# Kernel tuning notes

Hardware: AMD Instinct MI355X
Metric: run time of the kernel (lower is better)

## Reference

```python
import jax, jax.numpy as jnp
import numpy as np

B, C, NS, NT = 8, 256, 16384, 2048
KQ = 64            # self-attention key/query dim
D = 64             # cond_conv_feat_dim
W0, W1, W2 = D * D, D * D, D * 1   # dynamic weight sizes (predict_mask=True)
B0, B1, B2 = D, D, 1
CTRL = W0 + W1 + W2 + B0 + B1 + B2  # 8385


def setup_inputs() -> dict:
    key = jax.random.key(0)
    ks = jax.random.split(key, 9)
    return {
        "scene_feat": jax.random.normal(ks[0], (B, C, NS), jnp.float32),
        "template_feat": jax.random.normal(ks[1], (B, C, NT), jnp.float32),
        # SelfAttention 1x1-conv (= linear over channels) weights
        "q_w": jax.random.normal(ks[2], (KQ, C), jnp.float32) * 0.02,
        "k_w": jax.random.normal(ks[3], (KQ, C), jnp.float32) * 0.02,
        "v_w": jax.random.normal(ks[4], (C, C), jnp.float32) * 0.02,
        # projection head of SimpleAggregator: Conv1d(3*C -> D, k=1) + ReLU
        "proj_w": jax.random.normal(ks[5], (D, 3 * C), jnp.float32) * 0.02,
        "proj_b": jnp.zeros((D,), jnp.float32),
        # controller head: Linear(C -> CTRL), init normal(std=0.01), bias 0
        "ctrl_w": jax.random.normal(ks[6], (CTRL, C), jnp.float32) * 0.01,
        "ctrl_b": jnp.zeros((CTRL,), jnp.float32),
    }


def _self_attention(x, q_w, k_w, v_w):
    # x: [B, C, N] -> [B, C_out, N]
    q = jnp.einsum("kc,bcn->bnk", q_w, x)          # [B, N, KQ]
    k = jnp.einsum("kc,bcn->bkn", k_w, x)          # [B, KQ, N]
    v = jnp.einsum("oc,bcn->bno", v_w, x)          # [B, N, C_out]
    attn = jax.nn.softmax(jnp.einsum("bnk,bkm->bnm", q / jnp.sqrt(jnp.float32(KQ)), k), axis=-1)
    y = jnp.einsum("bnm,bmo->bon", attn, v)        # [B, C_out, N]
    return y


def reference(scene_feat, template_feat, q_w, k_w, v_w, proj_w, proj_b, ctrl_w, ctrl_b):
    # ---- SimpleAggregator (self-attention on template inside) ----
    t_sa = _self_attention(template_feat, q_w, k_w, v_w)       # [B, C, NT]
    t_max = jnp.max(t_sa, axis=-1, keepdims=True)              # [B, C, 1]
    aggr = jnp.concatenate(
        [scene_feat - t_max, scene_feat * t_max, scene_feat], axis=1
    )                                                          # [B, 3C, NS]
    x = jax.nn.relu(jnp.einsum("oc,bcn->bon", proj_w, aggr) + proj_b[None, :, None])  # [B, D, NS]

    # ---- controller head on ORIGINAL template_feat max-pooled ----
    pooled = jnp.max(template_feat, axis=-1)                   # [B, C]
    params = pooled @ ctrl_w.T + ctrl_b                        # [B, CTRL]

    # parse_dynamic_params: splits = weights then biases
    o = 0
    w0 = params[:, o:o + W0].reshape(B, D, D); o += W0
    w1 = params[:, o:o + W1].reshape(B, D, D); o += W1
    w2 = params[:, o:o + W2].reshape(B, 1, D); o += W2
    b0 = params[:, o:o + B0]; o += B0
    b1 = params[:, o:o + B1]; o += B1
    b2 = params[:, o:o + B2]

    # per-sample dynamic 1x1 convs (groups=batch trick == batched GEMM)
    x = jax.nn.relu(jnp.einsum("boi,bin->bon", w0, x) + b0[:, :, None])
    x = jax.nn.relu(jnp.einsum("boi,bin->bon", w1, x) + b1[:, :, None])
    x = jnp.einsum("boi,bin->bon", w2, x) + b2[:, :, None]    # [B, 1, NS], no relu (mask layer)
    return x.reshape(B, NS)
```

## Files before the change

### kernel.cpp

```cpp
#include <hip/hip_runtime.h>


typedef __attribute__((ext_vector_type(8))) short short8;
typedef __attribute__((ext_vector_type(4))) short short4v;
typedef __attribute__((ext_vector_type(4))) float f32x4;

__device__ __forceinline__ unsigned short f2bf(float f){
  unsigned u = __float_as_uint(f);
  u += 0x7FFFu + ((u >> 16) & 1u);
  return (unsigned short)(u >> 16);
}
__device__ __forceinline__ unsigned fenc(float f){
  unsigned u = __float_as_uint(f);
  return (u & 0x80000000u) ? ~u : (u | 0x80000000u);
}
__device__ __forceinline__ float fdec(unsigned k){
  unsigned u = (k & 0x80000000u) ? (k & 0x7FFFFFFFu) : ~k;
  return __uint_as_float(u);
}

__global__ __launch_bounds__(256) void k0w(const float* __restrict__ qw,
    const float* __restrict__ kw, const float* __restrict__ vw,
    unsigned short* __restrict__ Wbf, unsigned* __restrict__ tmaxe,
    unsigned* __restrict__ pooledEnc){
  if (blockIdx.x == 0){
    const unsigned ninf = fenc(-3.0e38f);
    for (int i = threadIdx.x; i < 2048; i += 256){
      tmaxe[i] = 0u;
      pooledEnc[i] = ninf;
    }
  }
  const int e = (blockIdx.x * 256 + threadIdx.x) * 4;
  const int row = e >> 8, c = e & 255;
  const float* src;
  float scl = 1.0f;
  if (row < 64){ src = qw + row * 256 + c; scl = 0.125f; }
  else if (row < 128){ src = kw + (row - 64) * 256 + c; }
  else { src = vw + (row - 128) * 256 + c; }
  float4 v = *(const float4*)src;
  short4v o;
  o[0] = (short)f2bf(v.x * scl); o[1] = (short)f2bf(v.y * scl);
  o[2] = (short)f2bf(v.z * scl); o[3] = (short)f2bf(v.w * scl);
  *(short4v*)(Wbf + e) = o;
}

__global__ __launch_bounds__(256) void k0_tt(const float* __restrict__ T,
    unsigned short* __restrict__ Tt, unsigned* __restrict__ pooledEnc){
  const int b = blockIdx.x, nt = blockIdx.y, ct = blockIdx.z;
  const int n0 = nt * 128, c0 = ct * 32;
  const int tid = threadIdx.x;
  __shared__ float Ls[32][129];
  const int cr = tid >> 3, nq = tid & 7;
  const float* src = T + ((size_t)b * 256 + c0 + cr) * 2048 + n0 + nq * 16;
  float4 v0 = ((const float4*)src)[0];
  float4 v1 = ((const float4*)src)[1];
  float4 v2 = ((const float4*)src)[2];
  float4 v3 = ((const float4*)src)[3];
  float mx = fmaxf(fmaxf(fmaxf(v0.x, v0.y), fmaxf(v0.z, v0.w)),
                   fmaxf(fmaxf(v1.x, v1.y), fmaxf(v1.z, v1.w)));
  mx = fmaxf(mx, fmaxf(fmaxf(fmaxf(v2.x, v2.y), fmaxf(v2.z, v2.w)),
                       fmaxf(fmaxf(v3.x, v3.y), fmaxf(v3.z, v3.w))));
  mx = fmaxf(mx, __shfl_xor(mx, 1));
  mx = fmaxf(mx, __shfl_xor(mx, 2));
  mx = fmaxf(mx, __shfl_xor(mx, 4));
  if (nq == 0) atomicMax(&pooledEnc[b * 256 + c0 + cr], fenc(mx));
  float* lr = &Ls[cr][nq * 16];
  *(float4*)lr = v0; *(float4*)(lr + 4) = v1;
  *(float4*)(lr + 8) = v2; *(float4*)(lr + 12) = v3;
  __syncthreads();
  const int nr = tid >> 1, ch = tid & 1;
  unsigned short ob[16];
  #pragma unroll
  for (int j = 0; j < 16; j++) ob[j] = f2bf(Ls[ch * 16 + j][nr]);
  unsigned short* dst = Tt + ((size_t)b * 2048 + n0 + nr) * 256 + c0 + ch * 16;
  *(short8*)dst = *(short8*)&ob[0];
  *(short8*)(dst + 8) = *(short8*)&ob[8];
}

__global__ __launch_bounds__(256) void k2_qkv(const unsigned short* __restrict__ Wbf,
    const unsigned short* __restrict__ Tt,
    unsigned short* __restrict__ qo, unsigned short* __restrict__ ko,
    unsigned short* __restrict__ vt){
  const int wg = blockIdx.x;
  const int b = wg & 7, nt = wg >> 3;
  const int n0 = nt * 32;
  const int tid = threadIdx.x, lane = tid & 63, w = tid >> 6;
  const int l15 = lane & 15, g = lane >> 4;
  const unsigned short* Tb = Tt + (size_t)b * 2048 * 256;

  f32x4 aqk[2][2], av[4][2];
  #pragma unroll
  for (int i = 0; i < 2; i++)
    #pragma unroll
    for (int nf = 0; nf < 2; nf++) aqk[i][nf] = (f32x4){0.f,0.f,0.f,0.f};
  #pragma unroll
  for (int j = 0; j < 4; j++)
    #pragma unroll
    for (int nf = 0; nf < 2; nf++) av[j][nf] = (f32x4){0.f,0.f,0.f,0.f};

  #pragma unroll 2
  for (int kc = 0; kc < 8; kc++){
    short8 bfr[2];
    #pragma unroll
    for (int nf = 0; nf < 2; nf++)
      bfr[nf] = *(const short8*)(Tb + (size_t)(n0 + nf * 16 + l15) * 256 + kc * 32 + g * 8);
    short8 aq[2];
    #pragma unroll
    for (int i = 0; i < 2; i++)
      aq[i] = *(const short8*)(Wbf + (size_t)((2 * w + i) * 16 + l15) * 256 + kc * 32 + g * 8);
    short8 afv[4];
    #pragma unroll
    for (int j = 0; j < 4; j++)
      afv[j] = *(const short8*)(Wbf + (size_t)(128 + (4 * w + j) * 16 + l15) * 256 + kc * 32 + g * 8);
    #pragma unroll
    for (int i = 0; i < 2; i++)
      #pragma unroll
      for (int nf = 0; nf < 2; nf++)
        aqk[i][nf] = __builtin_amdgcn_mfma_f32_16x16x32_bf16(aq[i], bfr[nf], aqk[i][nf], 0, 0, 0);
    #pragma unroll
    for (int j = 0; j < 4; j++)
      #pragma unroll
      for (int nf = 0; nf < 2; nf++)
        av[j][nf] = __builtin_amdgcn_mfma_f32_16x16x32_bf16(bfr[nf], afv[j], av[j][nf], 0, 0, 0);
  }
  unsigned short* qk = (w < 2) ? qo : ko;
  #pragma unroll
  for (int i = 0; i < 2; i++)
    #pragma unroll
    for (int nf = 0; nf < 2; nf++){
      int n = n0 + nf * 16 + l15;
      int cbase = (w & 1) * 32 + i * 16 + g * 4;
      short4v pk;
      #pragma unroll
      for (int r = 0; r < 4; r++) pk[r] = (short)f2bf(aqk[i][nf][r]);
      *(short4v*)(qk + ((size_t)b * 2048 + n) * 64 + cbase) = pk;
    }
  #pragma unroll
  for (int j = 0; j < 4; j++)
    #pragma unroll
    for (int nf = 0; nf < 2; nf++){
      int o = (4 * w + j) * 16 + l15;
      int nb2 = n0 + nf * 16 + g * 4;
      short4v pv;
      #pragma unroll
      for (int r = 0; r < 4; r++) pv[r] = (short)f2bf(av[j][nf][r]);
      *(short4v*)(vt + ((size_t)b * 256 + o) * 2048 + nb2) = pv;
    }
}

__global__ __launch_bounds__(256) void k3_params(const unsigned* __restrict__ pooledEnc,
    const float* __restrict__ cw, const float* __restrict__ cb,
    float* __restrict__ params){
  __shared__ float P[8 * 256];
  const int tid = threadIdx.x;
  for (int i = tid; i < 2048; i += 256) P[i] = fdec(pooledEnc[i]);
  __syncthreads();
  const int w = tid >> 6, lane = tid & 63;
  const int r = blockIdx.x * 4 + w;
  if (r >= 8385) return;
  float4 c4 = ((const float4*)(cw + (size_t)r * 256))[lane];
  float bias = cb[r];
  #pragma unroll
  for (int b = 0; b < 8; b++){
    const float* pbp = P + b * 256 + lane * 4;
    float s = c4.x * pbp[0] + c4.y * pbp[1] + c4.z * pbp[2] + c4.w * pbp[3];
    #pragma unroll
    for (int d = 1; d < 64; d <<= 1) s += __shfl_xor(s, d);
    if (lane == 0) params[b * 8385 + r] = s + bias;
  }
}

__global__ __launch_bounds__(512, 4) void kA_scores(
    const unsigned short* __restrict__ Qg, const unsigned short* __restrict__ Kg,
    unsigned short* __restrict__ Pg, float* __restrict__ sbuf,
    int b0, int bshift){
  const int wg = blockIdx.x;
  const int bmask = (1 << bshift) - 1;
  const int b = b0 + (wg & bmask);
  const int q0 = (wg >> bshift) * 32;
  const int qb0 = (wg >> bshift) * 2;
  const int tid = threadIdx.x, lane = tid & 63, w = tid >> 6;
  const int l15 = lane & 15, g = lane >> 4;
  __shared__ float wsum[32][8];
  const unsigned short* Qb = Qg + (size_t)b * 2048 * 64;
  const unsigned short* Kb = Kg + (size_t)b * 2048 * 64;
  unsigned short* Pb = Pg + (size_t)(wg & bmask) * 2048 * 2048;

  short8 qf[2][2];
  #pragma unroll
  for (int qi = 0; qi < 2; qi++)
    #pragma unroll
    for (int kc = 0; kc < 2; kc++)
      qf[qi][kc] = *(const short8*)(Qb + (size_t)(q0 + qi * 16 + l15) * 64 + kc * 32 + g * 8);

  float ps[2][4];
  #pragma unroll
  for (int qi = 0; qi < 2; qi++)
    #pragma unroll
    for (int r = 0; r < 4; r++) ps[qi][r] = 0.f;

  const int wm0 = w * 256;
  for (int mt = 0; mt < 4; ++mt){
    const int mb = wm0 + mt * 64;
    short8 kf[4][2];
    #pragma unroll
    for (int mi = 0; mi < 4; mi++)
      #pragma unroll
      for (int kc = 0; kc < 2; kc++)
        kf[mi][kc] = *(const short8*)(Kb + (size_t)(mb + mi * 16 + l15) * 64 + kc * 32 + g * 8);
    #pragma unroll
    for (int qi = 0; qi < 2; qi++){
      f32x4 sa[4];
      #pragma unroll
      for (int mi = 0; mi < 4; mi++) sa[mi] = (f32x4){0.f,0.f,0.f,0.f};
      #pragma unroll
      for (int mi = 0; mi < 4; mi++)
        #pragma unroll
        for (int kc = 0; kc < 2; kc++)
          sa[mi] = __builtin_amdgcn_mfma_f32_16x16x32_bf16(qf[qi][kc], kf[mi][kc], sa[mi], 0, 0, 0);
      #pragma unroll
      for (int mi = 0; mi < 4; mi++){
        short4v pk;
        #pragma unroll
        for (int r = 0; r < 4; r++){
          float p = __expf(sa[mi][r]);
          ps[qi][r] += p;
          pk[r] = (short)f2bf(p);
        }
        *(short4v*)(Pb + ((size_t)((qb0 + qi) * 128 + w * 16 + mt * 4 + mi)) * 256 + lane * 4) = pk;
      }
    }
  }
  #pragma unroll
  for (int qi = 0; qi < 2; qi++)
    #pragma unroll
    for (int r = 0; r < 4; r++){
      float t = ps[qi][r];
      t += __shfl_xor(t, 1); t += __shfl_xor(t, 2);
      t += __shfl_xor(t, 4); t += __shfl_xor(t, 8);
      if (l15 == 0) wsum[qi * 16 + g * 4 + r][w] = t;
    }
  __syncthreads();
  if (tid < 32){
    float t = 0.f;
    #pragma unroll
    for (int i = 0; i < 8; i++) t += wsum[tid][i];
    sbuf[(size_t)b * 2048 + q0 + tid] = t;
  }
}

__global__ __launch_bounds__(256, 2) void kB_pv(
    const unsigned short* __restrict__ Pg, const unsigned short* __restrict__ Vt,
    const float* __restrict__ sbuf, unsigned* __restrict__ tmaxe,
    int b0, int bshift){
  const int wg = blockIdx.x;
  const int bmask = (1 << bshift) - 1;
  const int b = b0 + (wg & bmask);
  const int rest = wg >> bshift;
  const int oh = rest & 1;
  const int n0 = (rest >> 1) * 64;
  const int qb0 = n0 >> 4;
  const int tid = threadIdx.x, lane = tid & 63, w = tid >> 6;
  const int l15 = lane & 15, g = lane >> 4;
  __shared__ __align__(16) unsigned char smem[24576];

  const unsigned short* Pb = Pg + (size_t)(wg & bmask) * 2048 * 2048;
  const unsigned short* Vb = Vt + ((size_t)b * 256 + oh * 128) * 2048;

  f32x4 acc[4][2];
  #pragma unroll
  for (int ni = 0; ni < 4; ni++)
    #pragma unroll
    for (int oi = 0; oi < 2; oi++) acc[ni][oi] = (f32x4){0.f,0.f,0.f,0.f};

  for (int m0 = 0; m0 < 2048; m0 += 64){
    const int mb0 = m0 >> 4;
    short8 stg[6];
    #pragma unroll
    for (int k = 0; k < 6; k++){
      int d = k * 4096 + tid * 16;
      if (k < 2){
        int ti = d >> 9;
        int qi = ti >> 2, mi = ti & 3;
        stg[k] = *(const short8*)(Pb + ((size_t)(qb0 + qi) * 128 + mb0 + mi) * 256 + ((d & 511) >> 1));
      } else {
        int dv = d - 8192;
        int row = dv >> 7;
        stg[k] = *(const short8*)(Vb + (size_t)row * 2048 + m0 + ((dv & 127) >> 1));
      }
    }
    __syncthreads();
    #pragma unroll
    for (int k = 0; k < 6; k++){
      int d = k * 4096 + tid * 16;
      if (k < 2){
        int ti = d >> 9;
        int qi = ti >> 2, mi = ti & 3;
        int lane0 = (d & 511) >> 3;
        #pragma unroll
        for (int idx = 0; idx < 8; idx++){
          int Lp = lane0 + (idx >> 2), r = idx & 3;
          int row = qi * 16 + ((Lp >> 4) << 2) + r;
          int col = mi * 16 + (Lp & 15);
          *(unsigned short*)(smem + ((row * 128 + col * 2) ^ ((row & 7) << 4))) =
              ((const unsigned short*)&stg[k])[idx];
        }
      } else {
        int dv = d - 8192;
        int row = dv >> 7;
        *(short8*)(smem + 8192 + (dv ^ ((row & 7) << 4))) = stg[k];
      }
    }
    __syncthreads();
    short8 af[4][2], bf[2][2];
    #pragma unroll
    for (int ni = 0; ni < 4; ni++)
      #pragma unroll
      for (int kc = 0; kc < 2; kc++){
        int row = ni * 16 + l15;
        af[ni][kc] = *(const short8*)(smem + ((row * 128 + kc * 64 + g * 16) ^ ((row & 7) << 4)));
      }
    #pragma unroll
    for (int oi = 0; oi < 2; oi++)
      #pragma unroll
      for (int kc = 0; kc < 2; kc++){
        int row = w * 32 + oi * 16 + l15;
        bf[oi][kc] = *(const short8*)(smem + 8192 + ((row * 128 + kc * 64 + g * 16) ^ ((row & 7) << 4)));
      }
    #pragma unroll
    for (int ni = 0; ni < 4; ni++)
      #pragma unroll
      for (int oi = 0; oi < 2; oi++)
        #pragma unroll
        for (int kc = 0; kc < 2; kc++)
          acc[ni][oi] = __builtin_amdgcn_mfma_f32_16x16x32_bf16(af[ni][kc], bf[oi][kc], acc[ni][oi], 0, 0, 0);
  }
  float inv[4][4];
  #pragma unroll
  for (int ni = 0; ni < 4; ni++)
    #pragma unroll
    for (int r = 0; r < 4; r++)
      inv[ni][r] = 1.0f / sbuf[(size_t)b * 2048 + n0 + ni * 16 + g * 4 + r];
  #pragma unroll
  for (int oi = 0; oi < 2; oi++){
    float cm = -1e30f;
    #pragma unroll
    for (int ni = 0; ni < 4; ni++)
      #pragma unroll
      for (int r = 0; r < 4; r++)
        cm = fmaxf(cm, acc[ni][oi][r] * inv[ni][r]);
    cm = fmaxf(cm, __shfl_xor(cm, 16));
    cm = fmaxf(cm, __shfl_xor(cm, 32));
    if (lane < 16)
      atomicMax(&tmaxe[b * 256 + oh * 128 + w * 32 + oi * 16 + lane], fenc(cm));
  }
}

__global__ __launch_bounds__(256) void k5_weff(const float* __restrict__ proj_w,
    const float* __restrict__ proj_b, const unsigned* __restrict__ tmaxe,
    const float* __restrict__ params, unsigned short* __restrict__ weff,
    float* __restrict__ beff, unsigned short* __restrict__ w0b,
    unsigned short* __restrict__ w1b){
  const int b = blockIdx.y, o = blockIdx.x;
  const int c = threadIdx.x;
  float t = fdec(tmaxe[b * 256 + c]);
  float p0 = proj_w[o * 768 + c];
  float p1 = proj_w[o * 768 + 256 + c];
  float p2 = proj_w[o * 768 + 512 + c];
  weff[((size_t)b * 64 + o) * 256 + c] = f2bf(p0 + p1 * t + p2);
  float s = p0 * t;
  #pragma unroll
  for (int d = 1; d < 64; d <<= 1) s += __shfl_xor(s, d);
  __shared__ float sm[4];
  if ((c & 63) == 0) sm[c >> 6] = s;
  __syncthreads();
  if (c == 0) beff[b * 64 + o] = proj_b[o] - (sm[0] + sm[1] + sm[2] + sm[3]);
  if (c < 64)        w0b[((size_t)b * 64 + o) * 64 + c] = f2bf(params[b * 8385 + o * 64 + c]);
  else if (c < 128)  w1b[((size_t)b * 64 + o) * 64 + (c - 64)] = f2bf(params[b * 8385 + 4096 + o * 64 + (c - 64)]);
}

__global__ __launch_bounds__(512) void k6_main(const float* __restrict__ Sg,
    const unsigned short* __restrict__ weff, const float* __restrict__ beff,
    const unsigned short* __restrict__ w0b, const unsigned short* __restrict__ w1b,
    const float* __restrict__ params, float* __restrict__ out){
  const int b = blockIdx.y, nt = blockIdx.x;
  const int n0 = nt * 256;
  const int tid = threadIdx.x, lane = tid & 63, w = tid >> 6;
  const int l15 = lane & 15, g = lane >> 4;
  __shared__ __align__(16) unsigned char smem[65536];
  unsigned short* H0 = (unsigned short*)smem;
  unsigned char*  Ub = smem + 32768;
  unsigned short* H1 = (unsigned short*)Ub;

  const float* Sb = Sg + (size_t)b * 256 * 16384;
  const unsigned short* We = weff + (size_t)b * 64 * 256;
  f32x4 a0[4][2];
  #pragma unroll
  for (int mi = 0; mi < 4; mi++)
    #pragma unroll
    for (int ni = 0; ni < 2; ni++) a0[mi][ni] = (f32x4){0.f,0.f,0.f,0.f};

  const int scc = tid & 31;
  const int snb = (tid >> 5) * 16;
  for (int k0 = 0; k0 < 256; k0 += 32){
    const float* src = Sb + (size_t)(k0 + scc) * 16384 + n0 + snb;
    float4 v0 = ((const float4*)src)[0];
    float4 v1 = ((const float4*)src)[1];
    float4 v2 = ((const float4*)src)[2];
    float4 v3 = ((const float4*)src)[3];
    float vals[16] = {v0.x,v0.y,v0.z,v0.w, v1.x,v1.y,v1.z,v1.w,
                      v2.x,v2.y,v2.z,v2.w, v3.x,v3.y,v3.z,v3.w};
    #pragma unroll
    for (int j = 0; j < 16; j++){
      int n = snb + j;
      unsigned byteo = ((unsigned)(n * 64 + scc * 2)) ^ ((unsigned)((n >> 1) & 3) << 4);
      *(unsigned short*)(Ub + byteo) = f2bf(vals[j]);
    }
    __syncthreads();
    short8 bf0[2];
    #pragma unroll
    for (int ni = 0; ni < 2; ni++){
      int n = w * 32 + ni * 16 + l15;
      bf0[ni] = *(const short8*)(Ub + (((unsigned)(n * 64 + g * 16)) ^ ((unsigned)((n >> 1) & 3) << 4)));
    }
    #pragma unroll
    for (int mi = 0; mi < 4; mi++){
      short8 af = *(const short8*)(We + (mi * 16 + l15) * 256 + k0 + g * 8);
      #pragma unroll
      for (int ni = 0; ni < 2; ni++)
        a0[mi][ni] = __builtin_amdgcn_mfma_f32_16x16x32_bf16(af, bf0[ni], a0[mi][ni], 0, 0, 0);
    }
    __syncthreads();
  }
  const float* be = beff + b * 64;
  #pragma unroll
  for (int mi = 0; mi < 4; mi++)
    #pragma unroll
    for (int ni = 0; ni < 2; ni++){
      int n = w * 32 + ni * 16 + l15;
      unsigned base = ((unsigned)(n * 128 + mi * 32 + g * 8)) ^ ((unsigned)((n & 7) << 4));
      unsigned short hh[4];
      #pragma unroll
      for (int r = 0; r < 4; r++){
        int o = mi * 16 + g * 4 + r;
        hh[r] = f2bf(fmaxf(a0[mi][ni][r] + be[o], 0.f));
      }
      *(unsigned*)((unsigned char*)H0 + base)     = (unsigned)hh[0] | ((unsigned)hh[1] << 16);
      *(unsigned*)((unsigned char*)H0 + base + 4) = (unsigned)hh[2] | ((unsigned)hh[3] << 16);
    }
  __syncthreads();
  f32x4 a1[4][2];
  #pragma unroll
  for (int mi = 0; mi < 4; mi++)
    #pragma unroll
    for (int ni = 0; ni < 2; ni++) a1[mi][ni] = (f32x4){0.f,0.f,0.f,0.f};
  const unsigned short* W0 = w0b + (size_t)b * 4096;
  #pragma unroll
  for (int ks = 0; ks < 2; ks++){
    short8 bfh[2];
    #pragma unroll
    for (int ni = 0; ni < 2; ni++){
      int n = w * 32 + ni * 16 + l15;
      unsigned off = ((unsigned)(n * 128 + ks * 64 + g * 16)) ^ ((unsigned)((n & 7) << 4));
      bfh[ni] = *(const short8*)((unsigned char*)H0 + off);
    }
    #pragma unroll
    for (int mi = 0; mi < 4; mi++){
      short8 af = *(const short8*)(W0 + (mi * 16 + l15) * 64 + ks * 32 + g * 8);
      #pragma unroll
      for (int ni = 0; ni < 2; ni++)
        a1[mi][ni] = __builtin_amdgcn_mfma_f32_16x16x32_bf16(af, bfh[ni], a1[mi][ni], 0, 0, 0);
    }
  }
  const float* pp = params + (size_t)b * 8385;
  const float* b0p = pp + 8256;
  #pragma unroll
  for (int mi = 0; mi < 4; mi++)
    #pragma unroll
    for (int ni = 0; ni < 2; ni++){
      int n = w * 32 + ni * 16 + l15;
      unsigned base = ((unsigned)(n * 128 + mi * 32 + g * 8)) ^ ((unsigned)((n & 7) << 4));
      unsigned short hh[4];
      #pragma unroll
      for (int r = 0; r < 4; r++){
        int o = mi * 16 + g * 4 + r;
        hh[r] = f2bf(fmaxf(a1[mi][ni][r] + b0p[o], 0.f));
      }
      *(unsigned*)((unsigned char*)H1 + base)     = (unsigned)hh[0] | ((unsigned)hh[1] << 16);
      *(unsigned*)((unsigned char*)H1 + base + 4) = (unsigned)hh[2] | ((unsigned)hh[3] << 16);
    }
  __syncthreads();
  f32x4 a2[4][2];
  #pragma unroll
  for (int mi = 0; mi < 4; mi++)
    #pragma unroll
    for (int ni = 0; ni < 2; ni++) a2[mi][ni] = (f32x4){0.f,0.f,0.f,0.f};
  const unsigned short* W1 = w1b + (size_t)b * 4096;
  #pragma unroll
  for (int ks = 0; ks < 2; ks++){
    short8 bfh[2];
    #pragma unroll
    for (int ni = 0; ni < 2; ni++){
      int n = w * 32 + ni * 16 + l15;
      unsigned off = ((unsigned)(n * 128 + ks * 64 + g * 16)) ^ ((unsigned)((n & 7) << 4));
      bfh[ni] = *(const short8*)((unsigned char*)H1 + off);
    }
    #pragma unroll
    for (int mi = 0; mi < 4; mi++){
      short8 af = *(const short8*)(W1 + (mi * 16 + l15) * 64 + ks * 32 + g * 8);
      #pragma unroll
      for (int ni = 0; ni < 2; ni++)
        a2[mi][ni] = __builtin_amdgcn_mfma_f32_16x16x32_bf16(af, bfh[ni], a2[mi][ni], 0, 0, 0);
    }
  }
  const float* b1p = pp + 8320;
  const float* w2p = pp + 8192;
  float b2v = pp[8384];
  #pragma unroll
  for (int ni = 0; ni < 2; ni++){
    float t = 0.f;
    #pragma unroll
    for (int mi = 0; mi < 4; mi++)
      #pragma unroll
      for (int r = 0; r < 4; r++){
        int o = mi * 16 + g * 4 + r;
        t += w2p[o] * fmaxf(a2[mi][ni][r] + b1p[o], 0.f);
      }
    t += __shfl_xor(t, 16);
    t += __shfl_xor(t, 32);
    if (lane < 16)
      out[(size_t)b * 16384 + n0 + w * 32 + ni * 16 + l15] = t + b2v;
  }
}

extern "C" void kernel_launch(void* const* d_in, const int* in_sizes, int n_in,
                              void* d_out, int out_size, void* d_ws, size_t ws_size,
                              hipStream_t stream){
  const float* scene = (const float*)d_in[0];
  const float* tmpl  = (const float*)d_in[1];
  const float* qw    = (const float*)d_in[2];
  const float* kw    = (const float*)d_in[3];
  const float* vw    = (const float*)d_in[4];
  const float* pw    = (const float*)d_in[5];
  const float* pb    = (const float*)d_in[6];
  const float* cw    = (const float*)d_in[7];
  const float* cb    = (const float*)d_in[8];
  float* out = (float*)d_out;
  char* ws = (char*)d_ws;

  unsigned short* Q      = (unsigned short*)(ws + 0);
  unsigned short* K      = (unsigned short*)(ws + (2u << 20));
  unsigned short* V      = (unsigned short*)(ws + (4u << 20));
  unsigned*       pooledEnc = (unsigned*)(ws + (12u << 20));
  unsigned*       tmaxe  = (unsigned*)(ws + (12u << 20) + 8192);
  float*          params = (float*)(ws + (12u << 20) + 16384);
  unsigned short* w0b    = (unsigned short*)(ws + (13u << 20));
  unsigned short* w1b    = (unsigned short*)(ws + (13u << 20) + 65536);
  unsigned short* weff   = (unsigned short*)(ws + (13u << 20) + 131072);
  float*          beff   = (float*)(ws + (13u << 20) + 131072 + 262144);
  float*          sbuf   = (float*)(ws + (14u << 20));
  unsigned short* Wbf    = (unsigned short*)(ws + (14u << 20) + 131072);
  unsigned short* Pbuf   = (unsigned short*)(ws + (16u << 20));
  unsigned short* Tt     = Pbuf;

  const size_t pPerBatch = (size_t)2048 * 2048 * 2;
  size_t avail = ws_size > (16u << 20) ? ws_size - (16u << 20) : 0;
  int nb = 8, bshift = 3;
  while (nb > 1 && (size_t)nb * pPerBatch > avail){ nb >>= 1; bshift--; }

  k0w<<<dim3(96), dim3(256), 0, stream>>>(qw, kw, vw, Wbf, tmaxe, pooledEnc);
  k0_tt<<<dim3(8, 16, 8), dim3(256), 0, stream>>>(tmpl, Tt, pooledEnc);
  k2_qkv<<<dim3(512), dim3(256), 0, stream>>>(Wbf, Tt, Q, K, V);
  k3_params<<<dim3(2097), dim3(256), 0, stream>>>(pooledEnc, cw, cb, params);
  for (int b0 = 0; b0 < 8; b0 += nb){
    kA_scores<<<dim3(64 * nb), dim3(512), 0, stream>>>(Q, K, Pbuf, sbuf, b0, bshift);
    kB_pv<<<dim3(64 * nb), dim3(256), 0, stream>>>(Pbuf, V, sbuf, tmaxe, b0, bshift);
  }
  k5_weff<<<dim3(64, 8), dim3(256), 0, stream>>>(pw, pb, tmaxe, params, weff, beff, w0b, w1b);
  k6_main<<<dim3(64, 8), dim3(512), 0, stream>>>(scene, weff, beff, w0b, w1b, params, out);
}
```

Baseline: 153.0 us.

## Double-buffer PV shared memory, merge QKV and params kernels, unroll scores loop

```diff
diff --git a/kernel.cpp b/kernel.cpp
--- a/kernel.cpp
+++ b/kernel.cpp
@@ -77,14 +77,34 @@
   *(short8*)(dst + 8) = *(short8*)&ob[8];
 }
 
-__global__ __launch_bounds__(256) void k2_qkv(const unsigned short* __restrict__ Wbf,
-    const unsigned short* __restrict__ Tt,
+__global__ __launch_bounds__(256) void k23_qkv_params(
+    const unsigned short* __restrict__ Wbf, const unsigned short* __restrict__ Tt,
     unsigned short* __restrict__ qo, unsigned short* __restrict__ ko,
-    unsigned short* __restrict__ vt){
+    unsigned short* __restrict__ vt,
+    const unsigned* __restrict__ pooledEnc, const float* __restrict__ cw,
+    const float* __restrict__ cb, float* __restrict__ params){
   const int wg = blockIdx.x;
+  const int tid = threadIdx.x, lane = tid & 63, w = tid >> 6;
+  if (wg >= 512){
+    __shared__ float P[8 * 256];
+    for (int i = tid; i < 2048; i += 256) P[i] = fdec(pooledEnc[i]);
+    __syncthreads();
+    const int r = (wg - 512) * 4 + w;
+    if (r >= 8385) return;
+    float4 c4 = ((const float4*)(cw + (size_t)r * 256))[lane];
+    float bias = cb[r];
+    #pragma unroll
+    for (int b = 0; b < 8; b++){
+      const float* pbp = P + b * 256 + lane * 4;
+      float s = c4.x * pbp[0] + c4.y * pbp[1] + c4.z * pbp[2] + c4.w * pbp[3];
+      #pragma unroll
+      for (int d = 1; d < 64; d <<= 1) s += __shfl_xor(s, d);
+      if (lane == 0) params[b * 8385 + r] = s + bias;
+    }
+    return;
+  }
   const int b = wg & 7, nt = wg >> 3;
   const int n0 = nt * 32;
-  const int tid = threadIdx.x, lane = tid & 63, w = tid >> 6;
   const int l15 = lane & 15, g = lane >> 4;
   const unsigned short* Tb = Tt + (size_t)b * 2048 * 256;
 
@@ -146,28 +166,6 @@
       for (int r = 0; r < 4; r++) pv[r] = (short)f2bf(av[j][nf][r]);
       *(short4v*)(vt + ((size_t)b * 256 + o) * 2048 + nb2) = pv;
     }
-}
-
-__global__ __launch_bounds__(256) void k3_params(const unsigned* __restrict__ pooledEnc,
-    const float* __restrict__ cw, const float* __restrict__ cb,
-    float* __restrict__ params){
-  __shared__ float P[8 * 256];
-  const int tid = threadIdx.x;
-  for (int i = tid; i < 2048; i += 256) P[i] = fdec(pooledEnc[i]);
-  __syncthreads();
-  const int w = tid >> 6, lane = tid & 63;
-  const int r = blockIdx.x * 4 + w;
-  if (r >= 8385) return;
-  float4 c4 = ((const float4*)(cw + (size_t)r * 256))[lane];
-  float bias = cb[r];
-  #pragma unroll
-  for (int b = 0; b < 8; b++){
-    const float* pbp = P + b * 256 + lane * 4;
-    float s = c4.x * pbp[0] + c4.y * pbp[1] + c4.z * pbp[2] + c4.w * pbp[3];
-    #pragma unroll
-    for (int d = 1; d < 64; d <<= 1) s += __shfl_xor(s, d);
-    if (lane == 0) params[b * 8385 + r] = s + bias;
-  }
 }
 
 __global__ __launch_bounds__(512, 4) void kA_scores(
@@ -200,6 +198,7 @@
     for (int r = 0; r < 4; r++) ps[qi][r] = 0.f;
 
   const int wm0 = w * 256;
+  #pragma unroll
   for (int mt = 0; mt < 4; ++mt){
     const int mb = wm0 + mt * 64;
     short8 kf[4][2];
@@ -262,7 +261,7 @@
   const int qb0 = n0 >> 4;
   const int tid = threadIdx.x, lane = tid & 63, w = tid >> 6;
   const int l15 = lane & 15, g = lane >> 4;
-  __shared__ __align__(16) unsigned char smem[24576];
+  __shared__ __align__(16) unsigned char smem[2][24576];
 
   const unsigned short* Pb = Pg + (size_t)(wg & bmask) * 2048 * 2048;
   const unsigned short* Vb = Vt + ((size_t)b * 256 + oh * 128) * 2048;
@@ -273,9 +272,9 @@
     #pragma unroll
     for (int oi = 0; oi < 2; oi++) acc[ni][oi] = (f32x4){0.f,0.f,0.f,0.f};
 
-  for (int m0 = 0; m0 < 2048; m0 += 64){
+  short8 stg[6];
+  auto LOADS = [&](int m0){
     const int mb0 = m0 >> 4;
-    short8 stg[6];
     #pragma unroll
     for (int k = 0; k < 6; k++){
       int d = k * 4096 + tid * 16;
@@ -289,7 +288,8 @@
         stg[k] = *(const short8*)(Vb + (size_t)row * 2048 + m0 + ((dv & 127) >> 1));
       }
     }
-    __syncthreads();
+  };
+  auto WRITES = [&](unsigned char* buf){
     #pragma unroll
     for (int k = 0; k < 6; k++){
       int d = k * 4096 + tid * 16;
@@ -302,30 +302,38 @@
           int Lp = lane0 + (idx >> 2), r = idx & 3;
           int row = qi * 16 + ((Lp >> 4) << 2) + r;
           int col = mi * 16 + (Lp & 15);
-          *(unsigned short*)(smem + ((row * 128 + col * 2) ^ ((row & 7) << 4))) =
+          *(unsigned short*)(buf + ((row * 128 + col * 2) ^ ((row & 7) << 4))) =
               ((const unsigned short*)&stg[k])[idx];
         }
       } else {
         int dv = d - 8192;
         int row = dv >> 7;
-        *(short8*)(smem + 8192 + (dv ^ ((row & 7) << 4))) = stg[k];
-      }
-    }
-    __syncthreads();
+        *(short8*)(buf + 8192 + (dv ^ ((row & 7) << 4))) = stg[k];
+      }
+    }
+  };
+
+  LOADS(0);
+  WRITES(smem[0]);
+  __syncthreads();
+
+  for (int t = 0; t < 32; ++t){
+    unsigned char* cur = smem[t & 1];
+    if (t < 31) LOADS((t + 1) * 64);
     short8 af[4][2], bf[2][2];
     #pragma unroll
     for (int ni = 0; ni < 4; ni++)
       #pragma unroll
       for (int kc = 0; kc < 2; kc++){
         int row = ni * 16 + l15;
-        af[ni][kc] = *(const short8*)(smem + ((row * 128 + kc * 64 + g * 16) ^ ((row & 7) << 4)));
+        af[ni][kc] = *(const short8*)(cur + ((row * 128 + kc * 64 + g * 16) ^ ((row & 7) << 4)));
       }
     #pragma unroll
     for (int oi = 0; oi < 2; oi++)
       #pragma unroll
       for (int kc = 0; kc < 2; kc++){
         int row = w * 32 + oi * 16 + l15;
-        bf[oi][kc] = *(const short8*)(smem + 8192 + ((row * 128 + kc * 64 + g * 16) ^ ((row & 7) << 4)));
+        bf[oi][kc] = *(const short8*)(cur + 8192 + ((row * 128 + kc * 64 + g * 16) ^ ((row & 7) << 4)));
       }
     #pragma unroll
     for (int ni = 0; ni < 4; ni++)
@@ -334,6 +342,10 @@
         #pragma unroll
         for (int kc = 0; kc < 2; kc++)
           acc[ni][oi] = __builtin_amdgcn_mfma_f32_16x16x32_bf16(af[ni][kc], bf[oi][kc], acc[ni][oi], 0, 0, 0);
+    if (t < 31){
+      WRITES(smem[(t + 1) & 1]);
+      __syncthreads();
+    }
   }
   float inv[4][4];
   #pragma unroll
@@ -570,8 +582,8 @@
 
   k0w<<<dim3(96), dim3(256), 0, stream>>>(qw, kw, vw, Wbf, tmaxe, pooledEnc);
   k0_tt<<<dim3(8, 16, 8), dim3(256), 0, stream>>>(tmpl, Tt, pooledEnc);
-  k2_qkv<<<dim3(512), dim3(256), 0, stream>>>(Wbf, Tt, Q, K, V);
-  k3_params<<<dim3(2097), dim3(256), 0, stream>>>(pooledEnc, cw, cb, params);
+  k23_qkv_params<<<dim3(512 + 2097), dim3(256), 0, stream>>>(Wbf, Tt, Q, K, V,
+                                                             pooledEnc, cw, cb, params);
   for (int b0 = 0; b0 < 8; b0 += nb){
     kA_scores<<<dim3(64 * nb), dim3(512), 0, stream>>>(Q, K, Pbuf, sbuf, b0, bshift);
     kB_pv<<<dim3(64 * nb), dim3(256), 0, stream>>>(Pbuf, V, sbuf, tmaxe, b0, bshift);
```

Result: no change. 151.5 us (-1.0%).
